# Performance work log

Hardware: AMD Instinct MI355X
Metric: run time of the kernel (lower is better)

## Reference

```python
import jax, jax.numpy as jnp
import numpy as np

N, H, G = 8192, 256, 256


def setup_inputs() -> dict:
    key = jax.random.key(0)
    ks = jax.random.split(key, 12)
    s = 1.0 / np.sqrt(H)
    inp = {
        "x": jax.random.normal(ks[0], (N, H), dtype=jnp.float32),
        "batch": jnp.sort(jax.random.randint(ks[1], (N,), 0, G)),
        "num_graphs": G,
        "aw": jax.random.uniform(ks[2], (H, H), jnp.float32, -s, s),
        "ab": jax.random.uniform(ks[3], (H,), jnp.float32, -s, s),
        "p1w": jax.random.uniform(ks[4], (H, H), jnp.float32, -s, s),
        "p1b": jax.random.uniform(ks[5], (H,), jnp.float32, -s, s),
        "p2w": jax.random.uniform(ks[6], (H, H), jnp.float32, -s, s),
        "p2b": jax.random.uniform(ks[7], (H,), jnp.float32, -s, s),
        "r1w": jax.random.uniform(ks[8], (H, H), jnp.float32, -s, s),
        "r1b": jax.random.uniform(ks[9], (H,), jnp.float32, -s, s),
        "r2w": jax.random.uniform(ks[10], (H, H), jnp.float32, -s, s),
        "r2b": jax.random.uniform(ks[11], (H,), jnp.float32, -s, s),
    }
    return inp


def reference(x, batch, num_graphs, aw, ab, p1w, p1b, p2w, p2b, r1w, r1b, r2w, r2b):
    # phi: two Linear+ReLU layers
    h = jax.nn.relu(jax.nn.relu(x @ p1w + p1b) @ p2w + p2b)          # [N, H]
    s = h @ aw + ab                                                  # attention scores [N, H]
    dot = s @ s.T                                                    # [N, N]
    mask = (batch[:, None] == batch[None, :]).astype(dot.dtype)      # block-diagonal [N, N]
    # hand-rolled masked softmax exactly as in the torch module
    max_vals = jnp.max(dot * mask, axis=1, keepdims=True)            # [N, 1]
    masked_dot = (dot - max_vals) * mask
    e = jnp.exp(masked_dot)
    attn = e / jnp.sum(e * mask, axis=1, keepdims=True) * mask       # [N, N]
    x_weighted = attn @ h                                            # [N, H]
    x_agg = jax.ops.segment_sum(x_weighted, batch, num_segments=num_graphs)  # [G, H]
    # rho: two Linear+ReLU layers
    out = jax.nn.relu(jax.nn.relu(x_agg @ r1w + r1b) @ r2w + r2b)    # [G, H]
    return out
```

## Files before the change

### kernel.cpp

```cpp
#include <hip/hip_runtime.h>
#include <hip/hip_bf16.h>
#include <stdint.h>

#define NN 8192
#define HH 256
#define GG 256

typedef __bf16 bf16x8 __attribute__((ext_vector_type(8)));
typedef float f32x4 __attribute__((ext_vector_type(4)));
typedef unsigned short u16v8 __attribute__((ext_vector_type(8)));

__device__ __forceinline__ ushort f2bf(float f) {
  union { float f; uint32_t u; } v; v.f = f;
  uint32_t u = v.u;
  u += 0x7fffu + ((u >> 16) & 1u);
  return (ushort)(u >> 16);
}
__device__ __forceinline__ float bf2f(ushort h) {
  union { uint32_t u; float f; } v; v.u = ((uint32_t)h) << 16;
  return v.f;
}

__global__ __launch_bounds__(512) void k_prep(const float* __restrict__ p1w,
                                              const float* __restrict__ p2w,
                                              const float* __restrict__ aw,
                                              const float* __restrict__ r1w,
                                              const float* __restrict__ r2w,
                                              ushort* __restrict__ wT1,
                                              ushort* __restrict__ wT2,
                                              ushort* __restrict__ wTa,
                                              ushort* __restrict__ rK1,
                                              ushort* __restrict__ rK2) {
  int b = blockIdx.x, t = threadIdx.x;
  if (b < 48) {
    int mat = b >> 4, tile = b & 15;
    int tr = (tile >> 2) * 64, tc = (tile & 3) * 64;
    const float* w = mat == 0 ? p1w : mat == 1 ? p2w : aw;
    ushort* o = mat == 0 ? wT1 : mat == 1 ? wT2 : wTa;
    __shared__ float tileb[64][65];
    int rr = t >> 3, cg = (t & 7) * 8;
    const float* src = w + (size_t)(tr + rr) * HH + tc + cg;
    float4 v0 = *(const float4*)src;
    float4 v1 = *(const float4*)(src + 4);
    float* drow = &tileb[rr][cg];
    drow[0] = v0.x; drow[1] = v0.y; drow[2] = v0.z; drow[3] = v0.w;
    drow[4] = v1.x; drow[5] = v1.y; drow[6] = v1.z; drow[7] = v1.w;
    __syncthreads();
    int rn = t >> 3, kg = (t & 7) * 8;
    u16v8 a;
#pragma unroll
    for (int j = 0; j < 8; ++j) a[j] = f2bf(tileb[kg + j][rn]);
    *(u16v8*)(o + (size_t)(tc + rn) * HH + tr + kg) = a;
  } else {
    int eb = b - 48;
    const float* src = (eb < 8) ? r1w : r2w;
    ushort* dst = (eb < 8) ? rK1 : rK2;
    int sub = eb & 7;
#pragma unroll
    for (int it = 0; it < 2; ++it) {
      int base = sub * 8192 + it * 4096 + t * 8;
      float4 v0 = *(const float4*)(src + base);
      float4 v1 = *(const float4*)(src + base + 4);
      u16v8 o;
      o[0] = f2bf(v0.x); o[1] = f2bf(v0.y); o[2] = f2bf(v0.z); o[3] = f2bf(v0.w);
      o[4] = f2bf(v1.x); o[5] = f2bf(v1.y); o[6] = f2bf(v1.z); o[7] = f2bf(v1.w);
      *(u16v8*)(dst + base) = o;
    }
  }
}

__global__ __launch_bounds__(512, 1) void k_main(
    const float* __restrict__ x, const int* __restrict__ batch,
    const float* __restrict__ ab,
    const float* __restrict__ p1b, const float* __restrict__ p2b,
    const float* __restrict__ r1b, const float* __restrict__ r2b,
    const ushort* __restrict__ wT1, const ushort* __restrict__ wT2,
    const ushort* __restrict__ wTa,
    const ushort* __restrict__ rK1, const ushort* __restrict__ rK2,
    float* __restrict__ out) {
  __shared__ char smem[136320];
  ushort* wl   = (ushort*)smem;
  ushort* actA = (ushort*)(smem + 65536);
  ushort* actB = (ushort*)(smem + 98304);
  int*    bb   = (int*)(smem + 131072);
  int*    mm   = (int*)(smem + 132096);
  float*  colw = (float*)(smem + 132128);
  float*  xa   = (float*)(smem + 133152);
  float*  parts= (float*)(smem + 134176);

  const int g = blockIdx.x, tid = threadIdx.x;
  const int lane = tid & 63, wid = tid >> 6;
  const int l15 = lane & 15, q = lane >> 4, x7 = l15 & 7;

  if (tid < 256) bb[tid] = batch[tid * 32];
  if (tid == 0) { mm[0] = 256; mm[1] = 256; }
  __syncthreads();
  if (tid < 256) {
    int v = bb[tid];
    int pv = (tid == 0) ? -1 : bb[tid - 1];
    if (v >= g && pv < g) mm[0] = tid;
    if (v >= g + 1 && pv < g + 1) mm[1] = tid;
  }
  __syncthreads();
  {
    int which = -1, v = 0;
    if (tid < 32) { which = 2; v = g; }
    else if (tid >= 64 && tid < 96) { which = 3; v = g + 1; }
    if (which >= 0) {
      int B = mm[which - 2];
      int u = tid & 31;
      if (B == 0) { if (u == 0) mm[which] = 0; }
      else {
        int i = (B - 1) * 32 + 1 + u;
        if (i <= 8191 && batch[i] >= v && batch[i - 1] < v) mm[which] = i;
        if (B == 256 && u == 0 && batch[8191] < v) mm[which] = 8192;
      }
    }
  }
  __syncthreads();
  const int r0 = mm[2];
  int n = mm[3] - r0;
  if (n > 64) n = 64;
  const int nrt = (n + 15) >> 4;
  const int R = nrt * 16;

  for (int ch = tid; ch < R * 32; ch += 512) {
    int row = ch >> 5, c = ch & 31;
    int srow = r0 + row; if (srow > 8191) srow = 8191;
    const float* xp = x + (size_t)srow * HH + c * 8;
    float4 v0 = *(const float4*)xp;
    float4 v1 = *(const float4*)(xp + 4);
    u16v8 o;
    o[0] = f2bf(v0.x); o[1] = f2bf(v0.y); o[2] = f2bf(v0.z); o[3] = f2bf(v0.w);
    o[4] = f2bf(v1.x); o[5] = f2bf(v1.y); o[6] = f2bf(v1.z); o[7] = f2bf(v1.w);
    int dst = (ch & ~31) | (c ^ (row & 7));
    *(u16v8*)(actA + dst * 8) = o;
  }
  __syncthreads();

  for (int L = 0; L < 3; ++L) {
    const ushort* wt = (L == 0) ? wT1 : (L == 1) ? wT2 : wTa;
    const float* bias = (L == 0) ? p1b : (L == 1) ? p2b : ab;
    const int dorelu = (L < 2);
    const ushort* aIn = (L & 1) ? actB : actA;
    ushort* aOut = (L & 1) ? actA : actB;
    for (int half = 0; half < 2; ++half) {
      const ushort* base = wt + half * 32768;
#pragma unroll
      for (int it = 0; it < 8; ++it) {
        int chunk = it * 512 + tid;
        int row = chunk >> 5, c = chunk & 31;
        int srcc = (chunk & ~31) | (c ^ (row & 7));
        __builtin_amdgcn_global_load_lds(
            (const __attribute__((address_space(1))) uint32_t*)(base + srcc * 8),
            (__attribute__((address_space(3))) uint32_t*)(wl + chunk * 8),
            16, 0, 0);
      }
      __syncthreads();
      for (int t = wid; t < nrt * 8; t += 8) {
        int rt = t >> 3, ct = t & 7;
        f32x4 acc = {0.f, 0.f, 0.f, 0.f};
#pragma unroll
        for (int kk = 0; kk < 8; ++kk) {
          int kc = (kk * 4 + q) ^ x7;
          bf16x8 a  = *(const bf16x8*)(aIn + ((rt * 16 + l15) * 32 + kc) * 8);
          bf16x8 bf = *(const bf16x8*)(wl + ((ct * 16 + l15) * 32 + kc) * 8);
          acc = __builtin_amdgcn_mfma_f32_16x16x32_bf16(a, bf, acc, 0, 0, 0);
        }
        int col = half * 128 + ct * 16 + l15;
        float bv = bias[col];
#pragma unroll
        for (int i = 0; i < 4; ++i) {
          float vv = acc[i] + bv;
          if (dorelu) vv = fmaxf(vv, 0.f);
          int r = rt * 16 + q * 4 + i;
          int cc = (col >> 3) ^ (r & 7);
          aOut[(r * 32 + cc) * 8 + (col & 7)] = f2bf(vv);
        }
      }
      __syncthreads();
    }
  }

  if (tid < 256) colw[tid] = 0.f;
  __syncthreads();
  {
    const char* stc = (const char*)actB;
    if (wid < 4 && wid * 16 < n) {
      f32x4 acc0 = {0.f, 0.f, 0.f, 0.f};
      f32x4 acc1 = acc0, acc2 = acc0, acc3 = acc0;
      const int arow = wid * 16 + l15;
#pragma unroll
      for (int kk = 0; kk < 8; kk++) {
        int kc = ((kk * 4 + q) ^ x7) << 4;
        bf16x8 a  = *(const bf16x8*)(stc + arow * 512 + kc);
        bf16x8 b0 = *(const bf16x8*)(stc + l15 * 512 + kc);
        acc0 = __builtin_amdgcn_mfma_f32_16x16x32_bf16(a, b0, acc0, 0, 0, 0);
        if (n > 16) {
          bf16x8 b1 = *(const bf16x8*)(stc + (16 + l15) * 512 + kc);
          acc1 = __builtin_amdgcn_mfma_f32_16x16x32_bf16(a, b1, acc1, 0, 0, 0);
        }
        if (n > 32) {
          bf16x8 b2 = *(const bf16x8*)(stc + (32 + l15) * 512 + kc);
          acc2 = __builtin_amdgcn_mfma_f32_16x16x32_bf16(a, b2, acc2, 0, 0, 0);
        }
        if (n > 48) {
          bf16x8 b3 = *(const bf16x8*)(stc + (48 + l15) * 512 + kc);
          acc3 = __builtin_amdgcn_mfma_f32_16x16x32_bf16(a, b3, acc3, 0, 0, 0);
        }
      }
      float mi[4], e0[4], e1[4], e2[4], e3[4], inv[4];
#pragma unroll
      for (int i = 0; i < 4; i++) {
        float mmx = (l15 < n) ? acc0[i] : -1e30f;
        if (16 + l15 < n) mmx = fmaxf(mmx, acc1[i]);
        if (32 + l15 < n) mmx = fmaxf(mmx, acc2[i]);
        if (48 + l15 < n) mmx = fmaxf(mmx, acc3[i]);
        mi[i] = mmx;
      }
#pragma unroll
      for (int off = 1; off < 16; off <<= 1)
#pragma unroll
        for (int i = 0; i < 4; i++) mi[i] = fmaxf(mi[i], __shfl_xor(mi[i], off));
#pragma unroll
      for (int i = 0; i < 4; i++) {
        e0[i] = (l15 < n)      ? __expf(acc0[i] - mi[i]) : 0.f;
        e1[i] = (16 + l15 < n) ? __expf(acc1[i] - mi[i]) : 0.f;
        e2[i] = (32 + l15 < n) ? __expf(acc2[i] - mi[i]) : 0.f;
        e3[i] = (48 + l15 < n) ? __expf(acc3[i] - mi[i]) : 0.f;
        inv[i] = e0[i] + e1[i] + e2[i] + e3[i];
      }
#pragma unroll
      for (int off = 1; off < 16; off <<= 1)
#pragma unroll
        for (int i = 0; i < 4; i++) inv[i] += __shfl_xor(inv[i], off);
#pragma unroll
      for (int i = 0; i < 4; i++) inv[i] = 1.f / inv[i];
      float cs[4];
#pragma unroll
      for (int t = 0; t < 4; t++) {
        const float* et = t == 0 ? e0 : t == 1 ? e1 : t == 2 ? e2 : e3;
        float c4 = 0.f;
#pragma unroll
        for (int i = 0; i < 4; i++) {
          int row = wid * 16 + q * 4 + i;
          c4 += (row < n) ? et[i] * inv[i] : 0.f;
        }
        cs[t] = c4;
      }
#pragma unroll
      for (int t = 0; t < 4; t++) {
        cs[t] += __shfl_xor(cs[t], 16);
        cs[t] += __shfl_xor(cs[t], 32);
      }
      if (lane < 16) {
#pragma unroll
        for (int t = 0; t < 4; t++)
          if (t * 16 < n) atomicAdd(&colw[t * 16 + l15], cs[t]);
      }
    }
  }
  __syncthreads();

  {
    int c = tid & 255, half = tid >> 8;
    float agg = 0.f;
    for (int jj = half; jj < n; jj += 2) {
      int cc = (c >> 3) ^ (jj & 7);
      agg = fmaf(colw[jj], bf2f(actA[(jj * 32 + cc) * 8 + (c & 7)]), agg);
    }
    parts[half * 256 + c] = agg;
  }
  __syncthreads();
  if (tid < 256) xa[tid] = parts[tid] + parts[256 + tid];
  __syncthreads();

  {
    float* t1 = colw;
    const int col = tid & 255, half = tid >> 8;
    const int k0 = half * 128;
    float a0 = 0.f, a1 = 0.f, a2 = 0.f, a3 = 0.f;
    const ushort* wp = rK1 + (size_t)k0 * HH + col;
#pragma unroll 8
    for (int k = 0; k < 128; k += 4) {
      a0 = fmaf(xa[k0 + k],     bf2f(wp[(size_t)(k)     * HH]), a0);
      a1 = fmaf(xa[k0 + k + 1], bf2f(wp[(size_t)(k + 1) * HH]), a1);
      a2 = fmaf(xa[k0 + k + 2], bf2f(wp[(size_t)(k + 2) * HH]), a2);
      a3 = fmaf(xa[k0 + k + 3], bf2f(wp[(size_t)(k + 3) * HH]), a3);
    }
    parts[half * 256 + col] = (a0 + a1) + (a2 + a3);
    __syncthreads();
    if (tid < 256) t1[tid] = fmaxf(r1b[tid] + parts[tid] + parts[256 + tid], 0.f);
    __syncthreads();
    a0 = a1 = a2 = a3 = 0.f;
    const ushort* wp2 = rK2 + (size_t)k0 * HH + col;
#pragma unroll 8
    for (int k = 0; k < 128; k += 4) {
      a0 = fmaf(t1[k0 + k],     bf2f(wp2[(size_t)(k)     * HH]), a0);
      a1 = fmaf(t1[k0 + k + 1], bf2f(wp2[(size_t)(k + 1) * HH]), a1);
      a2 = fmaf(t1[k0 + k + 2], bf2f(wp2[(size_t)(k + 2) * HH]), a2);
      a3 = fmaf(t1[k0 + k + 3], bf2f(wp2[(size_t)(k + 3) * HH]), a3);
    }
    parts[half * 256 + col] = (a0 + a1) + (a2 + a3);
    __syncthreads();
    if (tid < 256)
      out[(size_t)g * HH + tid] = fmaxf(r2b[tid] + parts[tid] + parts[256 + tid], 0.f);
  }
}

extern "C" void kernel_launch(void* const* d_in, const int* in_sizes, int n_in,
                              void* d_out, int out_size, void* d_ws, size_t ws_size,
                              hipStream_t stream) {
  const float* x   = (const float*)d_in[0];
  const int* batch = (const int*)d_in[1];
  const float* aw  = (const float*)d_in[3];
  const float* ab  = (const float*)d_in[4];
  const float* p1w = (const float*)d_in[5];
  const float* p1b = (const float*)d_in[6];
  const float* p2w = (const float*)d_in[7];
  const float* p2b = (const float*)d_in[8];
  const float* r1w = (const float*)d_in[9];
  const float* r1b = (const float*)d_in[10];
  const float* r2w = (const float*)d_in[11];
  const float* r2b = (const float*)d_in[12];
  float* out = (float*)d_out;

  char* ws = (char*)d_ws;
  ushort* wT1 = (ushort*)(ws);
  ushort* wT2 = wT1 + 65536;
  ushort* wTa = wT2 + 65536;
  ushort* rK1 = wTa + 65536;
  ushort* rK2 = rK1 + 65536;

  k_prep<<<dim3(64), dim3(512), 0, stream>>>(p1w, p2w, aw, r1w, r2w,
                                             wT1, wT2, wTa, rK1, rK2);
  k_main<<<dim3(256), dim3(512), 0, stream>>>(x, batch, ab, p1b, p2b, r1b, r2b,
                                              wT1, wT2, wTa, rK1, rK2, out);
}
```

Before: 34.20 us.

## Double-buffer weight quarters and widen main kernel to 1024 threads

Raises the per-graph block from 512 to 1024 threads and splits each 256x256 weight matrix into four quarters. The quarters are double-buffered in LDS so the next quarter's global-to-LDS load overlaps the MFMA work on the current one. The softmax is split across 8 waves, each covering two column tiles, and the partial max and sum values are merged through shared memory. The aggregation and the rho MLP loops are split four ways instead of two. The risks are more barriers per layer (12 stages instead of 6), and with at most 64 rows many waves sit idle.

```diff
diff --git a/kernel.cpp b/kernel.cpp
--- a/kernel.cpp
+++ b/kernel.cpp
@@ -69,7 +69,21 @@
   }
 }
 
-__global__ __launch_bounds__(512, 1) void k_main(
+#define LOADQ(SRC, DST)                                                        \
+  {                                                                            \
+    _Pragma("unroll")                                                          \
+    for (int it_ = 0; it_ < 2; ++it_) {                                        \
+      int ch_ = it_ * 1024 + tid;                                              \
+      int rw_ = ch_ >> 5, c_ = ch_ & 31;                                       \
+      int sc_ = (ch_ & ~31) | (c_ ^ (rw_ & 7));                                \
+      __builtin_amdgcn_global_load_lds(                                        \
+          (const __attribute__((address_space(1))) uint32_t*)((SRC) + sc_ * 8),\
+          (__attribute__((address_space(3))) uint32_t*)((DST) + ch_ * 8),      \
+          16, 0, 0);                                                           \
+    }                                                                          \
+  }
+
+__global__ __launch_bounds__(1024) void k_main(
     const float* __restrict__ x, const int* __restrict__ batch,
     const float* __restrict__ ab,
     const float* __restrict__ p1b, const float* __restrict__ p2b,
@@ -78,8 +92,9 @@
     const ushort* __restrict__ wTa,
     const ushort* __restrict__ rK1, const ushort* __restrict__ rK2,
     float* __restrict__ out) {
-  __shared__ char smem[136320];
-  ushort* wl   = (ushort*)smem;
+  __shared__ char smem[139808];
+  ushort* wq0  = (ushort*)smem;
+  ushort* wq1  = (ushort*)(smem + 32768);
   ushort* actA = (ushort*)(smem + 65536);
   ushort* actB = (ushort*)(smem + 98304);
   int*    bb   = (int*)(smem + 131072);
@@ -87,6 +102,9 @@
   float*  colw = (float*)(smem + 132128);
   float*  xa   = (float*)(smem + 133152);
   float*  parts= (float*)(smem + 134176);
+  float*  pmax = (float*)(smem + 138272);
+  float*  psum = (float*)(smem + 138784);
+  float*  fct  = (float*)(smem + 139296);
 
   const int g = blockIdx.x, tid = threadIdx.x;
   const int lane = tid & 63, wid = tid >> 6;
@@ -124,7 +142,10 @@
   const int nrt = (n + 15) >> 4;
   const int R = nrt * 16;
 
-  for (int ch = tid; ch < R * 32; ch += 512) {
+  LOADQ(wT1, wq0);
+  LOADQ(wT1 + 16384, wq1);
+
+  for (int ch = tid; ch < R * 32; ch += 1024) {
     int row = ch >> 5, c = ch & 31;
     int srow = r0 + row; if (srow > 8191) srow = 8191;
     const float* xp = x + (size_t)srow * HH + c * 8;
@@ -138,173 +159,173 @@
   }
   __syncthreads();
 
-  for (int L = 0; L < 3; ++L) {
-    const ushort* wt = (L == 0) ? wT1 : (L == 1) ? wT2 : wTa;
+  for (int s = 0; s < 12; ++s) {
+    const int L = s >> 2, qd = s & 3;
+    const ushort* cur = (s & 1) ? wq1 : wq0;
+    if (s >= 1 && s < 11) {
+      int sn = s + 1;
+      int Ln = sn >> 2, qn = sn & 3;
+      const ushort* wtn = (Ln == 0) ? wT1 : (Ln == 1) ? wT2 : wTa;
+      ushort* dstb = (sn & 1) ? wq1 : wq0;
+      LOADQ(wtn + qn * 16384, dstb);
+    }
+    const ushort* aIn = (L & 1) ? actB : actA;
+    ushort* aOut = (L & 1) ? actA : actB;
     const float* bias = (L == 0) ? p1b : (L == 1) ? p2b : ab;
     const int dorelu = (L < 2);
-    const ushort* aIn = (L & 1) ? actB : actA;
-    ushort* aOut = (L & 1) ? actA : actB;
-    for (int half = 0; half < 2; ++half) {
-      const ushort* base = wt + half * 32768;
-#pragma unroll
-      for (int it = 0; it < 8; ++it) {
-        int chunk = it * 512 + tid;
-        int row = chunk >> 5, c = chunk & 31;
-        int srcc = (chunk & ~31) | (c ^ (row & 7));
-        __builtin_amdgcn_global_load_lds(
-            (const __attribute__((address_space(1))) uint32_t*)(base + srcc * 8),
-            (__attribute__((address_space(3))) uint32_t*)(wl + chunk * 8),
-            16, 0, 0);
-      }
-      __syncthreads();
-      for (int t = wid; t < nrt * 8; t += 8) {
-        int rt = t >> 3, ct = t & 7;
-        f32x4 acc = {0.f, 0.f, 0.f, 0.f};
-#pragma unroll
-        for (int kk = 0; kk < 8; ++kk) {
-          int kc = (kk * 4 + q) ^ x7;
-          bf16x8 a  = *(const bf16x8*)(aIn + ((rt * 16 + l15) * 32 + kc) * 8);
-          bf16x8 bf = *(const bf16x8*)(wl + ((ct * 16 + l15) * 32 + kc) * 8);
-          acc = __builtin_amdgcn_mfma_f32_16x16x32_bf16(a, bf, acc, 0, 0, 0);
-        }
-        int col = half * 128 + ct * 16 + l15;
-        float bv = bias[col];
-#pragma unroll
-        for (int i = 0; i < 4; ++i) {
-          float vv = acc[i] + bv;
-          if (dorelu) vv = fmaxf(vv, 0.f);
-          int r = rt * 16 + q * 4 + i;
-          int cc = (col >> 3) ^ (r & 7);
-          aOut[(r * 32 + cc) * 8 + (col & 7)] = f2bf(vv);
-        }
-      }
-      __syncthreads();
-    }
+    if (wid < nrt * 4) {
+      int rt = wid >> 2, ct = wid & 3;
+      f32x4 acc = {0.f, 0.f, 0.f, 0.f};
+#pragma unroll
+      for (int kk = 0; kk < 8; ++kk) {
+        int kc = (kk * 4 + q) ^ x7;
+        bf16x8 a  = *(const bf16x8*)(aIn + ((rt * 16 + l15) * 32 + kc) * 8);
+        bf16x8 bf = *(const bf16x8*)(cur + ((ct * 16 + l15) * 32 + kc) * 8);
+        acc = __builtin_amdgcn_mfma_f32_16x16x32_bf16(a, bf, acc, 0, 0, 0);
+      }
+      int col = qd * 64 + ct * 16 + l15;
+      float bv = bias[col];
+#pragma unroll
+      for (int i = 0; i < 4; ++i) {
+        float vv = acc[i] + bv;
+        if (dorelu) vv = fmaxf(vv, 0.f);
+        int r = rt * 16 + q * 4 + i;
+        int cc = (col >> 3) ^ (r & 7);
+        aOut[(r * 32 + cc) * 8 + (col & 7)] = f2bf(vv);
+      }
+    }
+    __syncthreads();
   }
 
   if (tid < 256) colw[tid] = 0.f;
   __syncthreads();
-  {
+  const int rt = wid & 3, h2 = wid >> 2;
+  const bool liveW = (wid < 8) && (rt * 16 < n);
+  float e0[4], e1[4];
+  int cb0 = 0, cb1 = 0;
+  if (liveW) {
     const char* stc = (const char*)actB;
-    if (wid < 4 && wid * 16 < n) {
-      f32x4 acc0 = {0.f, 0.f, 0.f, 0.f};
-      f32x4 acc1 = acc0, acc2 = acc0, acc3 = acc0;
-      const int arow = wid * 16 + l15;
+    cb0 = (h2 * 2 + 0) * 16; cb1 = (h2 * 2 + 1) * 16;
+    f32x4 acc0 = {0.f, 0.f, 0.f, 0.f}, acc1 = acc0;
+    const int arow = rt * 16 + l15;
+    if (cb0 < n) {
 #pragma unroll
       for (int kk = 0; kk < 8; kk++) {
         int kc = ((kk * 4 + q) ^ x7) << 4;
         bf16x8 a  = *(const bf16x8*)(stc + arow * 512 + kc);
-        bf16x8 b0 = *(const bf16x8*)(stc + l15 * 512 + kc);
+        bf16x8 b0 = *(const bf16x8*)(stc + (cb0 + l15) * 512 + kc);
         acc0 = __builtin_amdgcn_mfma_f32_16x16x32_bf16(a, b0, acc0, 0, 0, 0);
-        if (n > 16) {
-          bf16x8 b1 = *(const bf16x8*)(stc + (16 + l15) * 512 + kc);
+        if (cb1 < n) {
+          bf16x8 b1 = *(const bf16x8*)(stc + (cb1 + l15) * 512 + kc);
           acc1 = __builtin_amdgcn_mfma_f32_16x16x32_bf16(a, b1, acc1, 0, 0, 0);
         }
-        if (n > 32) {
-          bf16x8 b2 = *(const bf16x8*)(stc + (32 + l15) * 512 + kc);
-          acc2 = __builtin_amdgcn_mfma_f32_16x16x32_bf16(a, b2, acc2, 0, 0, 0);
-        }
-        if (n > 48) {
-          bf16x8 b3 = *(const bf16x8*)(stc + (48 + l15) * 512 + kc);
-          acc3 = __builtin_amdgcn_mfma_f32_16x16x32_bf16(a, b3, acc3, 0, 0, 0);
-        }
-      }
-      float mi[4], e0[4], e1[4], e2[4], e3[4], inv[4];
+      }
+    }
+    float pm[4], ps[4];
+#pragma unroll
+    for (int i = 0; i < 4; i++) {
+      float mmx = (cb0 + l15 < n) ? acc0[i] : -1e30f;
+      if (cb1 + l15 < n) mmx = fmaxf(mmx, acc1[i]);
+      pm[i] = mmx;
+    }
+#pragma unroll
+    for (int off = 1; off < 16; off <<= 1)
+#pragma unroll
+      for (int i = 0; i < 4; i++) pm[i] = fmaxf(pm[i], __shfl_xor(pm[i], off));
+#pragma unroll
+    for (int i = 0; i < 4; i++) {
+      e0[i] = (cb0 + l15 < n) ? __expf(acc0[i] - pm[i]) : 0.f;
+      e1[i] = (cb1 + l15 < n) ? __expf(acc1[i] - pm[i]) : 0.f;
+      ps[i] = e0[i] + e1[i];
+    }
+#pragma unroll
+    for (int off = 1; off < 16; off <<= 1)
+#pragma unroll
+      for (int i = 0; i < 4; i++) ps[i] += __shfl_xor(ps[i], off);
+    if (l15 == 0) {
 #pragma unroll
       for (int i = 0; i < 4; i++) {
-        float mmx = (l15 < n) ? acc0[i] : -1e30f;
-        if (16 + l15 < n) mmx = fmaxf(mmx, acc1[i]);
-        if (32 + l15 < n) mmx = fmaxf(mmx, acc2[i]);
-        if (48 + l15 < n) mmx = fmaxf(mmx, acc3[i]);
-        mi[i] = mmx;
-      }
-#pragma unroll
-      for (int off = 1; off < 16; off <<= 1)
-#pragma unroll
-        for (int i = 0; i < 4; i++) mi[i] = fmaxf(mi[i], __shfl_xor(mi[i], off));
-#pragma unroll
-      for (int i = 0; i < 4; i++) {
-        e0[i] = (l15 < n)      ? __expf(acc0[i] - mi[i]) : 0.f;
-        e1[i] = (16 + l15 < n) ? __expf(acc1[i] - mi[i]) : 0.f;
-        e2[i] = (32 + l15 < n) ? __expf(acc2[i] - mi[i]) : 0.f;
-        e3[i] = (48 + l15 < n) ? __expf(acc3[i] - mi[i]) : 0.f;
-        inv[i] = e0[i] + e1[i] + e2[i] + e3[i];
-      }
-#pragma unroll
-      for (int off = 1; off < 16; off <<= 1)
-#pragma unroll
-        for (int i = 0; i < 4; i++) inv[i] += __shfl_xor(inv[i], off);
-#pragma unroll
-      for (int i = 0; i < 4; i++) inv[i] = 1.f / inv[i];
-      float cs[4];
-#pragma unroll
-      for (int t = 0; t < 4; t++) {
-        const float* et = t == 0 ? e0 : t == 1 ? e1 : t == 2 ? e2 : e3;
-        float c4 = 0.f;
-#pragma unroll
-        for (int i = 0; i < 4; i++) {
-          int row = wid * 16 + q * 4 + i;
-          c4 += (row < n) ? et[i] * inv[i] : 0.f;
-        }
-        cs[t] = c4;
-      }
-#pragma unroll
-      for (int t = 0; t < 4; t++) {
-        cs[t] += __shfl_xor(cs[t], 16);
-        cs[t] += __shfl_xor(cs[t], 32);
-      }
-      if (lane < 16) {
-#pragma unroll
-        for (int t = 0; t < 4; t++)
-          if (t * 16 < n) atomicAdd(&colw[t * 16 + l15], cs[t]);
-      }
+        int row = rt * 16 + q * 4 + i;
+        pmax[h2 * 64 + row] = pm[i];
+        psum[h2 * 64 + row] = ps[i];
+      }
+    }
+  }
+  __syncthreads();
+  if (tid < 128) {
+    int h = tid >> 6, row = tid & 63;
+    float m0 = pmax[row], m1 = pmax[64 + row];
+    float m = fmaxf(m0, m1);
+    float S = psum[row] * __expf(m0 - m) + psum[64 + row] * __expf(m1 - m);
+    fct[h * 64 + row] = (S > 0.f) ? __expf(pmax[h * 64 + row] - m) / S : 0.f;
+  }
+  __syncthreads();
+  if (liveW) {
+    float cs0 = 0.f, cs1 = 0.f;
+#pragma unroll
+    for (int i = 0; i < 4; i++) {
+      int row = rt * 16 + q * 4 + i;
+      if (row < n) {
+        float f = fct[h2 * 64 + row];
+        cs0 += e0[i] * f;
+        cs1 += e1[i] * f;
+      }
+    }
+    cs0 += __shfl_xor(cs0, 16); cs0 += __shfl_xor(cs0, 32);
+    cs1 += __shfl_xor(cs1, 16); cs1 += __shfl_xor(cs1, 32);
+    if (lane < 16) {
+      if (cb0 < n) atomicAdd(&colw[cb0 + l15], cs0);
+      if (cb1 < n) atomicAdd(&colw[cb1 + l15], cs1);
     }
   }
   __syncthreads();
 
   {
-    int c = tid & 255, half = tid >> 8;
+    int c = tid & 255, qr = tid >> 8;
     float agg = 0.f;
-    for (int jj = half; jj < n; jj += 2) {
+    for (int jj = qr; jj < n; jj += 4) {
       int cc = (c >> 3) ^ (jj & 7);
       agg = fmaf(colw[jj], bf2f(actA[(jj * 32 + cc) * 8 + (c & 7)]), agg);
     }
-    parts[half * 256 + c] = agg;
-  }
-  __syncthreads();
-  if (tid < 256) xa[tid] = parts[tid] + parts[256 + tid];
+    parts[qr * 256 + c] = agg;
+  }
+  __syncthreads();
+  if (tid < 256)
+    xa[tid] = (parts[tid] + parts[256 + tid]) + (parts[512 + tid] + parts[768 + tid]);
   __syncthreads();
 
   {
-    float* t1 = colw;
-    const int col = tid & 255, half = tid >> 8;
-    const int k0 = half * 128;
+    const int col = tid & 255, kq = tid >> 8;
+    const int k0 = kq * 64;
     float a0 = 0.f, a1 = 0.f, a2 = 0.f, a3 = 0.f;
     const ushort* wp = rK1 + (size_t)k0 * HH + col;
-#pragma unroll 8
-    for (int k = 0; k < 128; k += 4) {
+#pragma unroll 4
+    for (int k = 0; k < 64; k += 4) {
       a0 = fmaf(xa[k0 + k],     bf2f(wp[(size_t)(k)     * HH]), a0);
       a1 = fmaf(xa[k0 + k + 1], bf2f(wp[(size_t)(k + 1) * HH]), a1);
       a2 = fmaf(xa[k0 + k + 2], bf2f(wp[(size_t)(k + 2) * HH]), a2);
       a3 = fmaf(xa[k0 + k + 3], bf2f(wp[(size_t)(k + 3) * HH]), a3);
     }
-    parts[half * 256 + col] = (a0 + a1) + (a2 + a3);
-    __syncthreads();
-    if (tid < 256) t1[tid] = fmaxf(r1b[tid] + parts[tid] + parts[256 + tid], 0.f);
+    parts[kq * 256 + col] = (a0 + a1) + (a2 + a3);
+    __syncthreads();
+    if (tid < 256)
+      colw[tid] = fmaxf(r1b[tid] + (parts[tid] + parts[256 + tid]) +
+                        (parts[512 + tid] + parts[768 + tid]), 0.f);
     __syncthreads();
     a0 = a1 = a2 = a3 = 0.f;
     const ushort* wp2 = rK2 + (size_t)k0 * HH + col;
-#pragma unroll 8
-    for (int k = 0; k < 128; k += 4) {
-      a0 = fmaf(t1[k0 + k],     bf2f(wp2[(size_t)(k)     * HH]), a0);
-      a1 = fmaf(t1[k0 + k + 1], bf2f(wp2[(size_t)(k + 1) * HH]), a1);
-      a2 = fmaf(t1[k0 + k + 2], bf2f(wp2[(size_t)(k + 2) * HH]), a2);
-      a3 = fmaf(t1[k0 + k + 3], bf2f(wp2[(size_t)(k + 3) * HH]), a3);
-    }
-    parts[half * 256 + col] = (a0 + a1) + (a2 + a3);
+#pragma unroll 4
+    for (int k = 0; k < 64; k += 4) {
+      a0 = fmaf(colw[k0 + k],     bf2f(wp2[(size_t)(k)     * HH]), a0);
+      a1 = fmaf(colw[k0 + k + 1], bf2f(wp2[(size_t)(k + 1) * HH]), a1);
+      a2 = fmaf(colw[k0 + k + 2], bf2f(wp2[(size_t)(k + 2) * HH]), a2);
+      a3 = fmaf(colw[k0 + k + 3], bf2f(wp2[(size_t)(k + 3) * HH]), a3);
+    }
+    parts[kq * 256 + col] = (a0 + a1) + (a2 + a3);
     __syncthreads();
     if (tid < 256)
-      out[(size_t)g * HH + tid] = fmaxf(r2b[tid] + parts[tid] + parts[256 + tid], 0.f);
+      out[(size_t)g * HH + tid] = fmaxf(r2b[tid] + (parts[tid] + parts[256 + tid]) +
+                                        (parts[512 + tid] + parts[768 + tid]), 0.f);
   }
 }
 
@@ -334,6 +355,6 @@
 
   k_prep<<<dim3(64), dim3(512), 0, stream>>>(p1w, p2w, aw, r1w, r2w,
                                              wT1, wT2, wTa, rK1, rK2);
-  k_main<<<dim3(256), dim3(512), 0, stream>>>(x, batch, ab, p1b, p2b, r1b, r2b,
-                                              wT1, wT2, wTa, rK1, rK2, out);
-}
+  k_main<<<dim3(256), dim3(1024), 0, stream>>>(x, batch, ab, p1b, p2b, r1b, r2b,
+                                               wT1, wT2, wTa, rK1, rK2, out);
+}
```

New measurement: 33.26 us. 2.8% less time.

## Split per-graph fused kernel into row-parallel phi MLP and per-graph attention kernels

Applied to the files above, without the earlier changes.

Splits the single per-graph kernel into two. The first runs the phi MLP and score projection over 16-row tiles across 512 blocks, double-buffering K-slabs of the weights in LDS with global_load_lds, and writes h and s as bf16 to the workspace. The second kernel does the per-graph attention, aggregation and rho MLP, and adds a scalar fallback for graphs with more than 64 nodes. This spreads the MLP work across more CUs and no longer truncates large graphs. In exchange it adds a global round-trip for the intermediates and a third kernel launch.

```diff
diff --git a/kernel.cpp b/kernel.cpp
--- a/kernel.cpp
+++ b/kernel.cpp
@@ -50,7 +50,10 @@
     u16v8 a;
 #pragma unroll
     for (int j = 0; j < 8; ++j) a[j] = f2bf(tileb[kg + j][rn]);
-    *(u16v8*)(o + (size_t)(tc + rn) * HH + tr + kg) = a;
+    int col = tc + rn;
+    size_t idx = (size_t)(tr >> 6) * 16384 + (size_t)col * 64 +
+                 (size_t)((((kg >> 3) & 7) ^ (col & 7)) * 8);
+    *(u16v8*)(o + idx) = a;
   } else {
     int eb = b - 48;
     const float* src = (eb < 8) ? r1w : r2w;
@@ -69,33 +72,116 @@
   }
 }
 
-__global__ __launch_bounds__(512, 1) void k_main(
-    const float* __restrict__ x, const int* __restrict__ batch,
-    const float* __restrict__ ab,
-    const float* __restrict__ p1b, const float* __restrict__ p2b,
-    const float* __restrict__ r1b, const float* __restrict__ r2b,
+#define LOADSLAB(SRC, DST)                                                     \
+  {                                                                            \
+    _Pragma("unroll")                                                          \
+    for (int i_ = 0; i_ < 4; ++i_) {                                           \
+      int ch_ = i_ * 512 + tid;                                                \
+      __builtin_amdgcn_global_load_lds(                                        \
+          (const __attribute__((address_space(1))) uint32_t*)((SRC) + ch_ * 8),\
+          (__attribute__((address_space(3))) uint32_t*)((DST) + ch_ * 8),      \
+          16, 0, 0);                                                           \
+    }                                                                          \
+  }
+
+__global__ __launch_bounds__(512) void k_phi(
+    const float* __restrict__ x,
+    const float* __restrict__ ab, const float* __restrict__ p1b,
+    const float* __restrict__ p2b,
     const ushort* __restrict__ wT1, const ushort* __restrict__ wT2,
     const ushort* __restrict__ wTa,
+    ushort* __restrict__ hb, ushort* __restrict__ sb) {
+  __shared__ ushort s0[16384];
+  __shared__ ushort s1[16384];
+  __shared__ ushort act[4096];
+  const int tid = threadIdx.x;
+  const int rowbase = blockIdx.x * 16;
+  const int lane = tid & 63, wid = tid >> 6;
+  const int l15 = lane & 15, q = lane >> 4;
+  const int cw = wid * 32;
+
+  LOADSLAB(wT1, s0);
+
+  {
+    int row = tid >> 5, c = tid & 31;
+    const float* xp = x + (size_t)(rowbase + row) * HH + c * 8;
+    float4 v0 = *(const float4*)xp;
+    float4 v1 = *(const float4*)(xp + 4);
+    u16v8 o;
+    o[0] = f2bf(v0.x); o[1] = f2bf(v0.y); o[2] = f2bf(v0.z); o[3] = f2bf(v0.w);
+    o[4] = f2bf(v1.x); o[5] = f2bf(v1.y); o[6] = f2bf(v1.z); o[7] = f2bf(v1.w);
+    int dst = (tid & ~31) | (c ^ (row & 7));
+    *(u16v8*)(act + dst * 8) = o;
+  }
+  __syncthreads();
+
+  for (int L = 0; L < 3; ++L) {
+    f32x4 acc0 = {0.f, 0.f, 0.f, 0.f}, acc1 = acc0;
+#pragma unroll
+    for (int ks = 0; ks < 4; ++ks) {
+      const int s = L * 4 + ks;
+      const ushort* cur = (s & 1) ? s1 : s0;
+      if (s < 11) {
+        const int sn = s + 1;
+        const ushort* wtn = (sn >> 2) == 0 ? wT1 : (sn >> 2) == 1 ? wT2 : wTa;
+        ushort* dstb = (sn & 1) ? s1 : s0;
+        LOADSLAB(wtn + (sn & 3) * 16384, dstb);
+      }
+#pragma unroll
+      for (int kk = 0; kk < 2; ++kk) {
+        int c3 = kk * 4 + q;
+        int ca = (ks * 8 + c3) ^ (l15 & 7);
+        bf16x8 a = *(const bf16x8*)(act + (l15 * 32 + ca) * 8);
+        int col0 = cw + l15, col1 = cw + 16 + l15;
+        bf16x8 b0 = *(const bf16x8*)(cur + col0 * 64 + ((c3 ^ (col0 & 7)) * 8));
+        bf16x8 b1 = *(const bf16x8*)(cur + col1 * 64 + ((c3 ^ (col1 & 7)) * 8));
+        acc0 = __builtin_amdgcn_mfma_f32_16x16x32_bf16(a, b0, acc0, 0, 0, 0);
+        acc1 = __builtin_amdgcn_mfma_f32_16x16x32_bf16(a, b1, acc1, 0, 0, 0);
+      }
+      __syncthreads();
+    }
+    const float* bias = (L == 0) ? p1b : (L == 1) ? p2b : ab;
+#pragma unroll
+    for (int nt = 0; nt < 2; ++nt) {
+      f32x4 acc = nt ? acc1 : acc0;
+      int col = cw + nt * 16 + l15;
+      float bv = bias[col];
+#pragma unroll
+      for (int i = 0; i < 4; ++i) {
+        float vv = acc[i] + bv;
+        int r = q * 4 + i;
+        if (L < 2) {
+          vv = fmaxf(vv, 0.f);
+          act[(r * 32 + ((col >> 3) ^ (r & 7))) * 8 + (col & 7)] = f2bf(vv);
+          if (L == 1) hb[(size_t)(rowbase + r) * HH + col] = f2bf(vv);
+        } else {
+          sb[(size_t)(rowbase + r) * HH + ((col >> 3) ^ (r & 7)) * 8 + (col & 7)] =
+              f2bf(vv);
+        }
+      }
+    }
+    __syncthreads();
+  }
+}
+
+__global__ __launch_bounds__(256) void k_attn(
+    const ushort* __restrict__ sb, const ushort* __restrict__ hb,
+    const int* __restrict__ batch,
     const ushort* __restrict__ rK1, const ushort* __restrict__ rK2,
+    const float* __restrict__ r1b, const float* __restrict__ r2b,
     float* __restrict__ out) {
-  __shared__ char smem[136320];
-  ushort* wl   = (ushort*)smem;
-  ushort* actA = (ushort*)(smem + 65536);
-  ushort* actB = (ushort*)(smem + 98304);
-  int*    bb   = (int*)(smem + 131072);
-  int*    mm   = (int*)(smem + 132096);
-  float*  colw = (float*)(smem + 132128);
-  float*  xa   = (float*)(smem + 133152);
-  float*  parts= (float*)(smem + 134176);
-
+  __shared__ ushort st[64 * 256];
+  __shared__ float colw[256];
+  __shared__ float xa[256];
+  __shared__ float t1[256];
+  __shared__ int bb[256];
+  __shared__ int mm[4];
   const int g = blockIdx.x, tid = threadIdx.x;
-  const int lane = tid & 63, wid = tid >> 6;
-  const int l15 = lane & 15, q = lane >> 4, x7 = l15 & 7;
-
-  if (tid < 256) bb[tid] = batch[tid * 32];
+
+  bb[tid] = batch[tid * 32];
   if (tid == 0) { mm[0] = 256; mm[1] = 256; }
   __syncthreads();
-  if (tid < 256) {
+  {
     int v = bb[tid];
     int pv = (tid == 0) ? -1 : bb[tid - 1];
     if (v >= g && pv < g) mm[0] = tid;
@@ -120,79 +206,26 @@
   __syncthreads();
   const int r0 = mm[2];
   int n = mm[3] - r0;
-  if (n > 64) n = 64;
-  const int nrt = (n + 15) >> 4;
-  const int R = nrt * 16;
-
-  for (int ch = tid; ch < R * 32; ch += 512) {
-    int row = ch >> 5, c = ch & 31;
-    int srow = r0 + row; if (srow > 8191) srow = 8191;
-    const float* xp = x + (size_t)srow * HH + c * 8;
-    float4 v0 = *(const float4*)xp;
-    float4 v1 = *(const float4*)(xp + 4);
-    u16v8 o;
-    o[0] = f2bf(v0.x); o[1] = f2bf(v0.y); o[2] = f2bf(v0.z); o[3] = f2bf(v0.w);
-    o[4] = f2bf(v1.x); o[5] = f2bf(v1.y); o[6] = f2bf(v1.z); o[7] = f2bf(v1.w);
-    int dst = (ch & ~31) | (c ^ (row & 7));
-    *(u16v8*)(actA + dst * 8) = o;
-  }
-  __syncthreads();
-
-  for (int L = 0; L < 3; ++L) {
-    const ushort* wt = (L == 0) ? wT1 : (L == 1) ? wT2 : wTa;
-    const float* bias = (L == 0) ? p1b : (L == 1) ? p2b : ab;
-    const int dorelu = (L < 2);
-    const ushort* aIn = (L & 1) ? actB : actA;
-    ushort* aOut = (L & 1) ? actA : actB;
-    for (int half = 0; half < 2; ++half) {
-      const ushort* base = wt + half * 32768;
-#pragma unroll
-      for (int it = 0; it < 8; ++it) {
-        int chunk = it * 512 + tid;
-        int row = chunk >> 5, c = chunk & 31;
-        int srcc = (chunk & ~31) | (c ^ (row & 7));
-        __builtin_amdgcn_global_load_lds(
-            (const __attribute__((address_space(1))) uint32_t*)(base + srcc * 8),
-            (__attribute__((address_space(3))) uint32_t*)(wl + chunk * 8),
-            16, 0, 0);
-      }
-      __syncthreads();
-      for (int t = wid; t < nrt * 8; t += 8) {
-        int rt = t >> 3, ct = t & 7;
-        f32x4 acc = {0.f, 0.f, 0.f, 0.f};
-#pragma unroll
-        for (int kk = 0; kk < 8; ++kk) {
-          int kc = (kk * 4 + q) ^ x7;
-          bf16x8 a  = *(const bf16x8*)(aIn + ((rt * 16 + l15) * 32 + kc) * 8);
-          bf16x8 bf = *(const bf16x8*)(wl + ((ct * 16 + l15) * 32 + kc) * 8);
-          acc = __builtin_amdgcn_mfma_f32_16x16x32_bf16(a, bf, acc, 0, 0, 0);
-        }
-        int col = half * 128 + ct * 16 + l15;
-        float bv = bias[col];
-#pragma unroll
-        for (int i = 0; i < 4; ++i) {
-          float vv = acc[i] + bv;
-          if (dorelu) vv = fmaxf(vv, 0.f);
-          int r = rt * 16 + q * 4 + i;
-          int cc = (col >> 3) ^ (r & 7);
-          aOut[(r * 32 + cc) * 8 + (col & 7)] = f2bf(vv);
-        }
-      }
-      __syncthreads();
-    }
-  }
-
-  if (tid < 256) colw[tid] = 0.f;
-  __syncthreads();
-  {
-    const char* stc = (const char*)actB;
-    if (wid < 4 && wid * 16 < n) {
+  colw[tid] = 0.f;
+  const int lane = tid & 63, wid = tid >> 6;
+  const int l15 = lane & 15, q = lane >> 4;
+  const int x7g = (r0 + l15) & 7;
+
+  if (n <= 64) {
+    for (int ch = tid; ch < n * 32; ch += 256)
+      __builtin_amdgcn_global_load_lds(
+          (const __attribute__((address_space(1))) uint32_t*)(sb + ((size_t)r0 * 32 + ch) * 8),
+          (__attribute__((address_space(3))) uint32_t*)(st + ch * 8),
+          16, 0, 0);
+    __syncthreads();
+    const char* stc = (const char*)st;
+    if (wid * 16 < n) {
       f32x4 acc0 = {0.f, 0.f, 0.f, 0.f};
       f32x4 acc1 = acc0, acc2 = acc0, acc3 = acc0;
       const int arow = wid * 16 + l15;
 #pragma unroll
       for (int kk = 0; kk < 8; kk++) {
-        int kc = ((kk * 4 + q) ^ x7) << 4;
+        int kc = ((kk * 4 + q) ^ x7g) << 4;
         bf16x8 a  = *(const bf16x8*)(stc + arow * 512 + kc);
         bf16x8 b0 = *(const bf16x8*)(stc + l15 * 512 + kc);
         acc0 = __builtin_amdgcn_mfma_f32_16x16x32_bf16(a, b0, acc0, 0, 0, 0);
@@ -259,52 +292,79 @@
           if (t * 16 < n) atomicAdd(&colw[t * 16 + l15], cs[t]);
       }
     }
+    __syncthreads();
+  } else {
+    int nnn = n > 256 ? 256 : n;
+    __syncthreads();
+    for (int i = wid; i < nnn; i += 4) {
+      int ra = r0 + i;
+      const ushort* pa = sb + (size_t)ra * HH;
+      float d[4]; int j4[4];
+#pragma unroll
+      for (int u = 0; u < 4; u++) {
+        j4[u] = lane + u * 64;
+        d[u] = -1e30f;
+        if (j4[u] < nnn) {
+          int rb = r0 + j4[u];
+          const ushort* pb = sb + (size_t)rb * HH;
+          float acc = 0.f;
+          for (int c = 0; c < 32; ++c) {
+            int ca = c ^ (ra & 7), cb = c ^ (rb & 7);
+#pragma unroll
+            for (int e = 0; e < 8; ++e)
+              acc = fmaf(bf2f(pa[ca * 8 + e]), bf2f(pb[cb * 8 + e]), acc);
+          }
+          d[u] = acc;
+        }
+      }
+      float m = fmaxf(fmaxf(d[0], d[1]), fmaxf(d[2], d[3]));
+#pragma unroll
+      for (int off = 32; off; off >>= 1) m = fmaxf(m, __shfl_xor(m, off));
+      float e[4], ss = 0.f;
+#pragma unroll
+      for (int u = 0; u < 4; u++) { e[u] = (j4[u] < nnn) ? __expf(d[u] - m) : 0.f; ss += e[u]; }
+#pragma unroll
+      for (int off = 32; off; off >>= 1) ss += __shfl_xor(ss, off);
+      float iv = 1.f / ss;
+#pragma unroll
+      for (int u = 0; u < 4; u++)
+        if (j4[u] < nnn) atomicAdd(&colw[j4[u]], e[u] * iv);
+    }
+    __syncthreads();
+  }
+
+  {
+    int nn = n > 256 ? 256 : n;
+    float agg = 0.f;
+#pragma unroll 4
+    for (int j = 0; j < nn; ++j)
+      agg = fmaf(colw[j], bf2f(hb[(size_t)(r0 + j) * HH + tid]), agg);
+    xa[tid] = agg;
   }
   __syncthreads();
 
   {
-    int c = tid & 255, half = tid >> 8;
-    float agg = 0.f;
-    for (int jj = half; jj < n; jj += 2) {
-      int cc = (c >> 3) ^ (jj & 7);
-      agg = fmaf(colw[jj], bf2f(actA[(jj * 32 + cc) * 8 + (c & 7)]), agg);
-    }
-    parts[half * 256 + c] = agg;
-  }
-  __syncthreads();
-  if (tid < 256) xa[tid] = parts[tid] + parts[256 + tid];
-  __syncthreads();
-
-  {
-    float* t1 = colw;
-    const int col = tid & 255, half = tid >> 8;
-    const int k0 = half * 128;
     float a0 = 0.f, a1 = 0.f, a2 = 0.f, a3 = 0.f;
-    const ushort* wp = rK1 + (size_t)k0 * HH + col;
+    const ushort* wp = rK1 + tid;
 #pragma unroll 8
-    for (int k = 0; k < 128; k += 4) {
-      a0 = fmaf(xa[k0 + k],     bf2f(wp[(size_t)(k)     * HH]), a0);
-      a1 = fmaf(xa[k0 + k + 1], bf2f(wp[(size_t)(k + 1) * HH]), a1);
-      a2 = fmaf(xa[k0 + k + 2], bf2f(wp[(size_t)(k + 2) * HH]), a2);
-      a3 = fmaf(xa[k0 + k + 3], bf2f(wp[(size_t)(k + 3) * HH]), a3);
-    }
-    parts[half * 256 + col] = (a0 + a1) + (a2 + a3);
-    __syncthreads();
-    if (tid < 256) t1[tid] = fmaxf(r1b[tid] + parts[tid] + parts[256 + tid], 0.f);
+    for (int k = 0; k < HH; k += 4) {
+      a0 = fmaf(xa[k],     bf2f(wp[(size_t)(k)     * HH]), a0);
+      a1 = fmaf(xa[k + 1], bf2f(wp[(size_t)(k + 1) * HH]), a1);
+      a2 = fmaf(xa[k + 2], bf2f(wp[(size_t)(k + 2) * HH]), a2);
+      a3 = fmaf(xa[k + 3], bf2f(wp[(size_t)(k + 3) * HH]), a3);
+    }
+    t1[tid] = fmaxf(r1b[tid] + (a0 + a1) + (a2 + a3), 0.f);
     __syncthreads();
     a0 = a1 = a2 = a3 = 0.f;
-    const ushort* wp2 = rK2 + (size_t)k0 * HH + col;
+    const ushort* wp2 = rK2 + tid;
 #pragma unroll 8
-    for (int k = 0; k < 128; k += 4) {
-      a0 = fmaf(t1[k0 + k],     bf2f(wp2[(size_t)(k)     * HH]), a0);
-      a1 = fmaf(t1[k0 + k + 1], bf2f(wp2[(size_t)(k + 1) * HH]), a1);
-      a2 = fmaf(t1[k0 + k + 2], bf2f(wp2[(size_t)(k + 2) * HH]), a2);
-      a3 = fmaf(t1[k0 + k + 3], bf2f(wp2[(size_t)(k + 3) * HH]), a3);
-    }
-    parts[half * 256 + col] = (a0 + a1) + (a2 + a3);
-    __syncthreads();
-    if (tid < 256)
-      out[(size_t)g * HH + tid] = fmaxf(r2b[tid] + parts[tid] + parts[256 + tid], 0.f);
+    for (int k = 0; k < HH; k += 4) {
+      a0 = fmaf(t1[k],     bf2f(wp2[(size_t)(k)     * HH]), a0);
+      a1 = fmaf(t1[k + 1], bf2f(wp2[(size_t)(k + 1) * HH]), a1);
+      a2 = fmaf(t1[k + 2], bf2f(wp2[(size_t)(k + 2) * HH]), a2);
+      a3 = fmaf(t1[k + 3], bf2f(wp2[(size_t)(k + 3) * HH]), a3);
+    }
+    out[(size_t)g * HH + tid] = fmaxf(r2b[tid] + (a0 + a1) + (a2 + a3), 0.f);
   }
 }
 
@@ -326,7 +386,9 @@
   float* out = (float*)d_out;
 
   char* ws = (char*)d_ws;
-  ushort* wT1 = (ushort*)(ws);
+  ushort* hb  = (ushort*)(ws);
+  ushort* sb  = (ushort*)(ws + (size_t)4 * 1024 * 1024);
+  ushort* wT1 = (ushort*)(ws + (size_t)8 * 1024 * 1024);
   ushort* wT2 = wT1 + 65536;
   ushort* wTa = wT2 + 65536;
   ushort* rK1 = wTa + 65536;
@@ -334,6 +396,8 @@
 
   k_prep<<<dim3(64), dim3(512), 0, stream>>>(p1w, p2w, aw, r1w, r2w,
                                              wT1, wT2, wTa, rK1, rK2);
-  k_main<<<dim3(256), dim3(512), 0, stream>>>(x, batch, ab, p1b, p2b, r1b, r2b,
-                                              wT1, wT2, wTa, rK1, rK2, out);
-}
+  k_phi<<<dim3(512), dim3(512), 0, stream>>>(x, ab, p1b, p2b,
+                                             wT1, wT2, wTa, hb, sb);
+  k_attn<<<dim3(256), dim3(256), 0, stream>>>(sb, hb, batch, rK1, rK2,
+                                              r1b, r2b, out);
+}
```

Measured after the change: 38.31 us. +12.0%, slower.
